# Kernel tuning notes

Hardware: AMD Instinct MI355X
Metric: run time of the kernel (lower is better)

## Reference

```python
import jax, jax.numpy as jnp
import numpy as np

COUNT_BINS = 8
BOUND = 3.0
MIN_BIN_WIDTH = 1e-3
MIN_BIN_HEIGHT = 1e-3
MIN_DERIVATIVE = 1e-3
EPS = 1e-6


def _made_masks(D, H1, H2, M):
    indeg = np.arange(1, D + 1)                     # input degrees 1..D
    h1 = np.arange(H1) % (D - 1) + 1                # hidden degrees in [1, D-1]
    h2 = np.arange(H2) % (D - 1) + 1
    outdeg = np.tile(indeg, M)                      # (M*D,), reshape-compatible with (M, D)
    m1 = (h1[:, None] >= indeg[None, :]).astype(np.float32)   # (H1, D)
    m2 = (h2[:, None] >= h1[None, :]).astype(np.float32)      # (H2, H1)
    m3 = (outdeg[:, None] > h2[None, :]).astype(np.float32)   # (M*D, H2)
    return jnp.asarray(m1), jnp.asarray(m2), jnp.asarray(m3)


def _rq_spline_forward(x, w, h, d):
    # x: (B, D); w, h: (B, D, K) simplex weights; d: (B, D, K-1) softplus'd interior derivatives
    K = w.shape[-1]
    left, right = -BOUND, BOUND

    widths = MIN_BIN_WIDTH + (1.0 - MIN_BIN_WIDTH * K) * w
    heights = MIN_BIN_HEIGHT + (1.0 - MIN_BIN_HEIGHT * K) * h
    derivs = MIN_DERIVATIVE + d
    ones = jnp.ones_like(derivs[..., :1])
    derivs = jnp.concatenate([ones, derivs, ones], -1)          # (B, D, K+1), boundary slope 1

    cw = jnp.cumsum(widths, -1)
    edge_l = jnp.full_like(cw[..., :1], left)
    edge_r = jnp.full_like(cw[..., :1], right)
    cumw = jnp.concatenate([edge_l, left + (right - left) * cw[..., :-1], edge_r], -1)  # (B, D, K+1)
    widths = cumw[..., 1:] - cumw[..., :-1]
    ch = jnp.cumsum(heights, -1)
    cumh = jnp.concatenate([edge_l, left + (right - left) * ch[..., :-1], edge_r], -1)
    heights = cumh[..., 1:] - cumh[..., :-1]

    inside = (x >= left) & (x <= right)
    xc = jnp.clip(x, left, right)
    # pyro: bin_idx = sum(x >= cumwidths + eps) - 1
    idx = jnp.sum((xc[..., None] >= (cumw + EPS)).astype(jnp.int32), -1) - 1
    idx = jnp.clip(idx, 0, K - 1)                               # (B, D)

    def g(t):
        return jnp.take_along_axis(t, idx[..., None], axis=-1)[..., 0]

    x_k, w_k = g(cumw), g(widths)
    y_k, h_k = g(cumh), g(heights)
    delta = h_k / w_k
    d_k, d_k1 = g(derivs), g(derivs[..., 1:])

    theta = (xc - x_k) / w_k
    tt = theta * (1.0 - theta)
    num = h_k * (delta * theta ** 2 + d_k * tt)
    den = delta + (d_k + d_k1 - 2.0 * delta) * tt
    y = y_k + num / den
    dnum = delta ** 2 * (d_k1 * theta ** 2 + 2.0 * delta * tt + d_k * (1.0 - theta) ** 2)
    ld = jnp.log(dnum) - 2.0 * jnp.log(den)
    return jnp.where(inside, y, x), jnp.where(inside, ld, jnp.zeros_like(ld))


def _forward(x, W1, b1, W2, b2, W3, b3):
    B, D = x.shape
    H1, H2 = W1.shape[0], W2.shape[0]
    K = COUNT_BINS
    M = 3 * K - 1
    m1, m2, m3 = _made_masks(D, H1, H2, M)
    h1 = jax.nn.relu(x @ (W1 * m1).T + b1)
    h2 = jax.nn.relu(h1 @ (W2 * m2).T + b2)
    p = (h2 @ (W3 * m3).T + b3).reshape(B, M, D)                # (B, 3K-1, D)
    w = jax.nn.softmax(jnp.swapaxes(p[:, :K, :], 1, 2), axis=-1)          # (B, D, K)
    hgt = jax.nn.softmax(jnp.swapaxes(p[:, K:2 * K, :], 1, 2), axis=-1)   # (B, D, K)
    d = jax.nn.softplus(jnp.swapaxes(p[:, 2 * K:, :], 1, 2))              # (B, D, K-1)
    z, ld = _rq_spline_forward(x, w, hgt, d)
    return z, ld.sum(-1)


def setup_inputs() -> dict:
    key = jax.random.key(0)
    ks = jax.random.split(key, 7)
    B, D, H1, H2 = 32768, 64, 64, 32
    M = 3 * COUNT_BINS - 1
    s1, s2, s3 = 1.0 / np.sqrt(D), 1.0 / np.sqrt(H1), 1.0 / np.sqrt(H2)
    return {
        "x": jax.random.normal(ks[0], (B, D), jnp.float32),
        "W1": jax.random.uniform(ks[1], (H1, D), jnp.float32, -s1, s1),
        "b1": jax.random.uniform(ks[2], (H1,), jnp.float32, -s1, s1),
        "W2": jax.random.uniform(ks[3], (H2, H1), jnp.float32, -s2, s2),
        "b2": jax.random.uniform(ks[4], (H2,), jnp.float32, -s2, s2),
        "W3": jax.random.uniform(ks[5], (M * D, H2), jnp.float32, -s3, s3),
        "b3": jax.random.uniform(ks[6], (M * D,), jnp.float32, -s3, s3),
    }


def reference(x, W1, b1, W2, b2, W3, b3):
    return _forward(x, W1, b1, W2, b2, W3, b3)
```

## Files before the change

### kernel.cpp

```cpp
#include <hip/hip_runtime.h>

#define NM 23

typedef short short8 __attribute__((ext_vector_type(8)));
typedef float f32x4 __attribute__((ext_vector_type(4)));

__device__ __forceinline__ float softplus_f(float v) {
  return fmaxf(v, 0.f) + __logf(1.f + __expf(-fabsf(v)));
}

__device__ __forceinline__ float fastrcp(float v) {
  return __builtin_amdgcn_rcpf(v);
}

__device__ __forceinline__ unsigned short bf16_rne(float x) {
  unsigned u = __float_as_uint(x);
  u += 0x7FFFu + ((u >> 16) & 1u);
  return (unsigned short)(u >> 16);
}

__global__ __launch_bounds__(256) void prep_kernel(
    const float* __restrict__ W1, const float* __restrict__ W2,
    const float* __restrict__ W3,
    unsigned short* __restrict__ B1hi, unsigned short* __restrict__ B1lo,
    unsigned short* __restrict__ B2hi, unsigned short* __restrict__ B2lo,
    unsigned short* __restrict__ B3hi, unsigned short* __restrict__ B3lo) {
  const int idx = blockIdx.x * 256 + threadIdx.x;
  const int j = idx & 7, lane = (idx >> 3) & 63;
  const int col = lane & 15, quad = lane >> 4;

  if (idx < 4096) {
    const int rest = idx >> 9, kt = rest & 1, nt = rest >> 1;
    const int k = kt * 32 + quad * 8 + j;
    const int n = nt * 16 + col;
    const float v = ((n % 63) >= k) ? W1[n * 64 + k] : 0.f;
    const unsigned short h = bf16_rne(v);
    B1hi[idx] = h;
    B1lo[idx] = bf16_rne(v - __uint_as_float(((unsigned)h) << 16));
  }
  if (idx < 2048) {
    const int rest = idx >> 9, kt = rest & 1, nt = rest >> 1;
    const int k = kt * 32 + quad * 8 + j;
    const int n = nt * 16 + col;
    const float v = ((k % 63) <= n) ? W2[n * 64 + k] : 0.f;
    const unsigned short h = bf16_rne(v);
    B2hi[idx] = h;
    B2lo[idx] = bf16_rne(v - __uint_as_float(((unsigned)h) << 16));
  }
  if (idx < 92 * 64 * 8) {
    const int nt = idx >> 9;
    const int n = nt * 16 + col;
    const int d = n & 63;
    const int k = quad * 8 + j;
    const float v = (k < d) ? W3[(size_t)n * 32 + k] : 0.f;
    const unsigned short h = bf16_rne(v);
    B3hi[idx] = h;
    B3lo[idx] = bf16_rne(v - __uint_as_float(((unsigned)h) << 16));
  }
}

__device__ __forceinline__ void cvt_hilo(const float* src, short8& hi,
                                         short8& lo) {
  const f32x4 a0 = *reinterpret_cast<const f32x4*>(src);
  const f32x4 a1 = *reinterpret_cast<const f32x4*>(src + 4);
  const float af[8] = {a0.x, a0.y, a0.z, a0.w, a1.x, a1.y, a1.z, a1.w};
  #pragma unroll
  for (int j = 0; j < 8; ++j) {
    const unsigned short h = bf16_rne(af[j]);
    hi[j] = (short)h;
    lo[j] = (short)bf16_rne(af[j] - __uint_as_float(((unsigned)h) << 16));
  }
}

__global__ __launch_bounds__(256, 4) void fused_kernel(
    const float* __restrict__ x,
    const unsigned short* __restrict__ B1hi,
    const unsigned short* __restrict__ B1lo,
    const float* __restrict__ b1,
    const unsigned short* __restrict__ B2hi,
    const unsigned short* __restrict__ B2lo,
    const float* __restrict__ b2,
    const unsigned short* __restrict__ B3hi,
    const unsigned short* __restrict__ B3lo,
    const float* __restrict__ b3,
    float* __restrict__ out, int B) {
  __shared__ float xs[64][68];
  __shared__ float h2s[64][36];
  __shared__ float b3s[64 * NM];

  const int t = threadIdx.x;
  const int b0 = blockIdx.x * 64;

  #pragma unroll
  for (int u = 0; u < 4; ++u) {
    const int idx = t + u * 256;
    const int rr = idx >> 4, c4 = (idx & 15) * 4;
    const float4 v = *reinterpret_cast<const float4*>(
        x + (size_t)b0 * 64 + (size_t)idx * 4);
    xs[rr][c4 + 0] = v.x; xs[rr][c4 + 1] = v.y;
    xs[rr][c4 + 2] = v.z; xs[rr][c4 + 3] = v.w;
  }
  for (int idx = t; idx < 64 * NM; idx += 256) {
    const int dl = idx / NM, m = idx - dl * NM;
    b3s[idx] = b3[m * 64 + dl];
  }
  __syncthreads();

  const int lane = t & 63;
  const int wv   = __builtin_amdgcn_readfirstlane(t >> 6);
  const int mt   = wv;
  const int col  = lane & 15;
  const int quad = lane >> 4;
  const int arow = mt * 16 + col;
  const int row0 = mt * 16 + quad * 4;

  float xvv[4][4];
  #pragma unroll
  for (int dc = 0; dc < 4; ++dc)
    #pragma unroll
    for (int reg = 0; reg < 4; ++reg)
      xvv[dc][reg] = xs[row0 + reg][dc * 16 + col];

  {
    short8 ahi[2], alo[2];
    #pragma unroll
    for (int kt = 0; kt < 2; ++kt)
      cvt_hilo(&xs[arow][kt * 32 + quad * 8], ahi[kt], alo[kt]);

    #pragma unroll
    for (int nt = 0; nt < 4; ++nt) {
      const float bv = b1[nt * 16 + col];
      f32x4 acc = {bv, bv, bv, bv};
      #pragma unroll
      for (int kt = 0; kt < 2; ++kt) {
        const size_t off = ((size_t)(nt * 2 + kt) * 64 + lane) * 8;
        const short8 bh = *reinterpret_cast<const short8*>(B1hi + off);
        const short8 bl = *reinterpret_cast<const short8*>(B1lo + off);
        acc = __builtin_amdgcn_mfma_f32_16x16x32_bf16(ahi[kt], bh, acc, 0, 0, 0);
        acc = __builtin_amdgcn_mfma_f32_16x16x32_bf16(alo[kt], bh, acc, 0, 0, 0);
        acc = __builtin_amdgcn_mfma_f32_16x16x32_bf16(ahi[kt], bl, acc, 0, 0, 0);
      }
      #pragma unroll
      for (int reg = 0; reg < 4; ++reg)
        xs[row0 + reg][nt * 16 + col] = fmaxf(acc[reg], 0.f);
    }
  }

  {
    short8 ahi[2], alo[2];
    #pragma unroll
    for (int kt = 0; kt < 2; ++kt)
      cvt_hilo(&xs[arow][kt * 32 + quad * 8], ahi[kt], alo[kt]);

    #pragma unroll
    for (int nt = 0; nt < 2; ++nt) {
      const float bv = b2[nt * 16 + col];
      f32x4 acc = {bv, bv, bv, bv};
      #pragma unroll
      for (int kt = 0; kt < 2; ++kt) {
        const size_t off = ((size_t)(nt * 2 + kt) * 64 + lane) * 8;
        const short8 bh = *reinterpret_cast<const short8*>(B2hi + off);
        const short8 bl = *reinterpret_cast<const short8*>(B2lo + off);
        acc = __builtin_amdgcn_mfma_f32_16x16x32_bf16(ahi[kt], bh, acc, 0, 0, 0);
        acc = __builtin_amdgcn_mfma_f32_16x16x32_bf16(alo[kt], bh, acc, 0, 0, 0);
        acc = __builtin_amdgcn_mfma_f32_16x16x32_bf16(ahi[kt], bl, acc, 0, 0, 0);
      }
      #pragma unroll
      for (int reg = 0; reg < 4; ++reg)
        h2s[row0 + reg][nt * 16 + col] = fmaxf(acc[reg], 0.f);
    }
  }

  short8 ahi, alo;
  cvt_hilo(&h2s[arow][quad * 8], ahi, alo);

  float ldr[4] = {0.f, 0.f, 0.f, 0.f};
  const float WSC = 1.0f - 1e-3f * 8.0f;

  #pragma unroll 1
  for (int dc = 0; dc < 4; ++dc) {
    const int d = dc * 16 + col;

    float xcv[4], fidx[4], xkv[4], wkv[4], ykv[4], hkv[4];

    {
      f32x4 acc[8];
      #pragma unroll
      for (int m = 0; m < 8; ++m) {
        const float bv = b3s[d * NM + m];
        acc[m] = (f32x4){bv, bv, bv, bv};
      }
      #pragma unroll
      for (int m = 0; m < 8; ++m) {
        const size_t off = ((size_t)(4 * m + dc) * 64 + lane) * 8;
        const short8 bh = *reinterpret_cast<const short8*>(B3hi + off);
        const short8 bl = *reinterpret_cast<const short8*>(B3lo + off);
        acc[m] = __builtin_amdgcn_mfma_f32_16x16x32_bf16(ahi, bh, acc[m], 0, 0, 0);
        acc[m] = __builtin_amdgcn_mfma_f32_16x16x32_bf16(alo, bh, acc[m], 0, 0, 0);
        acc[m] = __builtin_amdgcn_mfma_f32_16x16x32_bf16(ahi, bl, acc[m], 0, 0, 0);
      }
      #pragma unroll
      for (int reg = 0; reg < 4; ++reg) {
        float ew[8], sw = 0.f;
        #pragma unroll
        for (int k = 0; k < 8; ++k) { ew[k] = __expf(acc[k][reg]); sw += ew[k]; }
        const float invw = fastrcp(sw);
        float cumw[9];
        cumw[0] = -3.f;
        float cw = 0.f;
        #pragma unroll
        for (int k = 0; k < 7; ++k) {
          cw += 1e-3f + WSC * (ew[k] * invw);
          cumw[k + 1] = fmaf(6.f, cw, -3.f);
        }
        cumw[8] = 3.f;

        const float xv = xvv[dc][reg];
        const float xc = fminf(fmaxf(xv, -3.f), 3.f);
        float fi = 0.f, xk = cumw[0], xk1 = cumw[1];
        #pragma unroll
        for (int k = 1; k < 8; ++k) {
          const bool s = xc >= cumw[k] + 1e-6f;
          xk  = s ? cumw[k]     : xk;
          xk1 = s ? cumw[k + 1] : xk1;
          fi  = s ? (float)k    : fi;
        }
        xcv[reg] = xc; fidx[reg] = fi; xkv[reg] = xk; wkv[reg] = xk1 - xk;
      }
    }

    {
      f32x4 acc[8];
      #pragma unroll
      for (int m = 0; m < 8; ++m) {
        const float bv = b3s[d * NM + (8 + m)];
        acc[m] = (f32x4){bv, bv, bv, bv};
      }
      #pragma unroll
      for (int m = 0; m < 8; ++m) {
        const size_t off = ((size_t)(4 * (8 + m) + dc) * 64 + lane) * 8;
        const short8 bh = *reinterpret_cast<const short8*>(B3hi + off);
        const short8 bl = *reinterpret_cast<const short8*>(B3lo + off);
        acc[m] = __builtin_amdgcn_mfma_f32_16x16x32_bf16(ahi, bh, acc[m], 0, 0, 0);
        acc[m] = __builtin_amdgcn_mfma_f32_16x16x32_bf16(alo, bh, acc[m], 0, 0, 0);
        acc[m] = __builtin_amdgcn_mfma_f32_16x16x32_bf16(ahi, bl, acc[m], 0, 0, 0);
      }
      #pragma unroll
      for (int reg = 0; reg < 4; ++reg) {
        float eh[8], sh = 0.f;
        #pragma unroll
        for (int k = 0; k < 8; ++k) { eh[k] = __expf(acc[k][reg]); sh += eh[k]; }
        const float invh = fastrcp(sh);
        float cumh[9];
        cumh[0] = -3.f;
        float ch = 0.f;
        #pragma unroll
        for (int k = 0; k < 7; ++k) {
          ch += 1e-3f + WSC * (eh[k] * invh);
          cumh[k + 1] = fmaf(6.f, ch, -3.f);
        }
        cumh[8] = 3.f;

        float yk = cumh[0], yk1 = cumh[1];
        #pragma unroll
        for (int k = 1; k < 8; ++k) {
          const bool s = fidx[reg] >= (float)k;
          yk  = s ? cumh[k]     : yk;
          yk1 = s ? cumh[k + 1] : yk1;
        }
        ykv[reg] = yk; hkv[reg] = yk1 - yk;
      }
    }

    {
      f32x4 acc[7];
      #pragma unroll
      for (int m = 0; m < 7; ++m) {
        const float bv = b3s[d * NM + (16 + m)];
        acc[m] = (f32x4){bv, bv, bv, bv};
      }
      #pragma unroll
      for (int m = 0; m < 7; ++m) {
        const size_t off = ((size_t)(4 * (16 + m) + dc) * 64 + lane) * 8;
        const short8 bh = *reinterpret_cast<const short8*>(B3hi + off);
        const short8 bl = *reinterpret_cast<const short8*>(B3lo + off);
        acc[m] = __builtin_amdgcn_mfma_f32_16x16x32_bf16(ahi, bh, acc[m], 0, 0, 0);
        acc[m] = __builtin_amdgcn_mfma_f32_16x16x32_bf16(alo, bh, acc[m], 0, 0, 0);
        acc[m] = __builtin_amdgcn_mfma_f32_16x16x32_bf16(ahi, bl, acc[m], 0, 0, 0);
      }
      #pragma unroll
      for (int reg = 0; reg < 4; ++reg) {
        float p[7];
        #pragma unroll
        for (int k = 0; k < 7; ++k) p[k] = acc[k][reg];
        const float fi = fidx[reg];

        float pa = p[0], pb = p[0];
        #pragma unroll
        for (int k = 2; k < 8; ++k) pa = (fi >= (float)k) ? p[k - 1] : pa;
        #pragma unroll
        for (int k = 1; k < 7; ++k) pb = (fi >= (float)k) ? p[k] : pb;
        const float spa = 1e-3f + softplus_f(pa);
        const float spb = 1e-3f + softplus_f(pb);
        const float dk  = (fi >= 0.5f) ? spa : 1.f;
        const float dk1 = (fi >= 6.5f) ? 1.f : spb;

        const float xc = xcv[reg], xk = xkv[reg], wk = wkv[reg];
        const float yk = ykv[reg], hk = hkv[reg];
        const float invwk = fastrcp(wk);
        const float delta = hk * invwk;
        const float theta = (xc - xk) * invwk;
        const float omt = 1.f - theta;
        const float tt = theta * omt;
        const float th2 = theta * theta;
        const float num = hk * (delta * th2 + dk * tt);
        const float den = delta + (dk + dk1 - 2.f * delta) * tt;
        const float rden = fastrcp(den);
        const float yv = yk + num * rden;
        const float dnum =
            delta * delta * (dk1 * th2 + 2.f * delta * tt + dk * omt * omt);
        const float ldv = __logf(dnum * rden * rden);

        const float xv = xvv[dc][reg];
        const bool inside = (xv >= -3.f) && (xv <= 3.f);
        xs[row0 + reg][d] = inside ? yv : xv;
        ldr[reg] += inside ? ldv : 0.f;
      }
    }
  }

  #pragma unroll
  for (int mask = 1; mask <= 8; mask <<= 1) {
    #pragma unroll
    for (int reg = 0; reg < 4; ++reg)
      ldr[reg] += __shfl_xor(ldr[reg], mask, 64);
  }

  if (col == 0) {
    #pragma unroll
    for (int reg = 0; reg < 4; ++reg)
      out[(size_t)B * 64 + b0 + row0 + reg] = ldr[reg];
  }

  __syncthreads();

  #pragma unroll
  for (int u = 0; u < 4; ++u) {
    const int idx = t + u * 256;
    const int rr = idx >> 4, c4 = (idx & 15) * 4;
    const float4 v = make_float4(xs[rr][c4 + 0], xs[rr][c4 + 1],
                                 xs[rr][c4 + 2], xs[rr][c4 + 3]);
    *reinterpret_cast<float4*>(out + (size_t)(b0 + rr) * 64 + c4) = v;
  }
}

extern "C" void kernel_launch(void* const* d_in, const int* in_sizes, int n_in,
                              void* d_out, int out_size, void* d_ws, size_t ws_size,
                              hipStream_t stream) {
  const float* x  = (const float*)d_in[0];
  const float* W1 = (const float*)d_in[1];
  const float* b1 = (const float*)d_in[2];
  const float* W2 = (const float*)d_in[3];
  const float* b2 = (const float*)d_in[4];
  const float* W3 = (const float*)d_in[5];
  const float* b3 = (const float*)d_in[6];
  float* out = (float*)d_out;
  char* ws   = (char*)d_ws;

  unsigned short* B1hi = (unsigned short*)(ws);
  unsigned short* B1lo = (unsigned short*)(ws + 8192);
  unsigned short* B2hi = (unsigned short*)(ws + 16384);
  unsigned short* B2lo = (unsigned short*)(ws + 20480);
  unsigned short* B3hi = (unsigned short*)(ws + 24576);
  unsigned short* B3lo = (unsigned short*)(ws + 118784);

  const int B = in_sizes[0] / 64;

  prep_kernel<<<184, 256, 0, stream>>>(W1, W2, W3, B1hi, B1lo, B2hi, B2lo,
                                       B3hi, B3lo);

  fused_kernel<<<B / 64, 256, 0, stream>>>(
      x, B1hi, B1lo, b1, B2hi, B2lo, b2, B3hi, B3lo, b3, out, B);
}
```

Measured before the change: 117.5 us.

## Split spline feature dimension across two blocks per row tile with logdet reduce kernel

Launches twice as many blocks: each block recomputes layers 1-2 for its 64 rows but handles only half of the 64 output features in the costly layer-3 and spline stage. Per-half log-determinants go to a workspace and are summed by a new small reduce kernel. The aim is more parallelism and a shorter per-block tail, at the cost of doing the first two layers twice, reading x twice, and an extra launch.

```diff
diff --git a/kernel.cpp b/kernel.cpp
--- a/kernel.cpp
+++ b/kernel.cpp
@@ -83,13 +83,16 @@
     const unsigned short* __restrict__ B3hi,
     const unsigned short* __restrict__ B3lo,
     const float* __restrict__ b3,
-    float* __restrict__ out, int B) {
+    float* __restrict__ out, float* __restrict__ ldws, int B) {
   __shared__ float xs[64][68];
   __shared__ float h2s[64][36];
-  __shared__ float b3s[64 * NM];
+  __shared__ float b3s[32 * NM];
 
   const int t = threadIdx.x;
-  const int b0 = blockIdx.x * 64;
+  const int bid = blockIdx.x;
+  const int ds = (bid >> 3) & 1;
+  const int rb = ((bid >> 4) << 3) | (bid & 7);
+  const int b0 = rb * 64;
 
   #pragma unroll
   for (int u = 0; u < 4; ++u) {
@@ -100,9 +103,9 @@
     xs[rr][c4 + 0] = v.x; xs[rr][c4 + 1] = v.y;
     xs[rr][c4 + 2] = v.z; xs[rr][c4 + 3] = v.w;
   }
-  for (int idx = t; idx < 64 * NM; idx += 256) {
+  for (int idx = t; idx < 32 * NM; idx += 256) {
     const int dl = idx / NM, m = idx - dl * NM;
-    b3s[idx] = b3[m * 64 + dl];
+    b3s[idx] = b3[m * 64 + ds * 32 + dl];
   }
   __syncthreads();
 
@@ -114,12 +117,12 @@
   const int arow = mt * 16 + col;
   const int row0 = mt * 16 + quad * 4;
 
-  float xvv[4][4];
-  #pragma unroll
-  for (int dc = 0; dc < 4; ++dc)
+  float xvv[2][4];
+  #pragma unroll
+  for (int dcl = 0; dcl < 2; ++dcl)
     #pragma unroll
     for (int reg = 0; reg < 4; ++reg)
-      xvv[dc][reg] = xs[row0 + reg][dc * 16 + col];
+      xvv[dcl][reg] = xs[row0 + reg][ds * 32 + dcl * 16 + col];
 
   {
     short8 ahi[2], alo[2];
@@ -178,8 +181,9 @@
   const float WSC = 1.0f - 1e-3f * 8.0f;
 
   #pragma unroll 1
-  for (int dc = 0; dc < 4; ++dc) {
-    const int d = dc * 16 + col;
+  for (int dcl = 0; dcl < 2; ++dcl) {
+    const int dc = ds * 2 + dcl;
+    const int dl = dcl * 16 + col;
 
     float xcv[4], fidx[4], xkv[4], wkv[4], ykv[4], hkv[4];
 
@@ -187,7 +191,7 @@
       f32x4 acc[8];
       #pragma unroll
       for (int m = 0; m < 8; ++m) {
-        const float bv = b3s[d * NM + m];
+        const float bv = b3s[dl * NM + m];
         acc[m] = (f32x4){bv, bv, bv, bv};
       }
       #pragma unroll
@@ -215,7 +219,7 @@
         }
         cumw[8] = 3.f;
 
-        const float xv = xvv[dc][reg];
+        const float xv = xvv[dcl][reg];
         const float xc = fminf(fmaxf(xv, -3.f), 3.f);
         float fi = 0.f, xk = cumw[0], xk1 = cumw[1];
         #pragma unroll
@@ -233,7 +237,7 @@
       f32x4 acc[8];
       #pragma unroll
       for (int m = 0; m < 8; ++m) {
-        const float bv = b3s[d * NM + (8 + m)];
+        const float bv = b3s[dl * NM + (8 + m)];
         acc[m] = (f32x4){bv, bv, bv, bv};
       }
       #pragma unroll
@@ -276,7 +280,7 @@
       f32x4 acc[7];
       #pragma unroll
       for (int m = 0; m < 7; ++m) {
-        const float bv = b3s[d * NM + (16 + m)];
+        const float bv = b3s[dl * NM + (16 + m)];
         acc[m] = (f32x4){bv, bv, bv, bv};
       }
       #pragma unroll
@@ -321,9 +325,9 @@
             delta * delta * (dk1 * th2 + 2.f * delta * tt + dk * omt * omt);
         const float ldv = __logf(dnum * rden * rden);
 
-        const float xv = xvv[dc][reg];
+        const float xv = xvv[dcl][reg];
         const bool inside = (xv >= -3.f) && (xv <= 3.f);
-        xs[row0 + reg][d] = inside ? yv : xv;
+        h2s[row0 + reg][dl] = inside ? yv : xv;
         ldr[reg] += inside ? ldv : 0.f;
       }
     }
@@ -339,19 +343,26 @@
   if (col == 0) {
     #pragma unroll
     for (int reg = 0; reg < 4; ++reg)
-      out[(size_t)B * 64 + b0 + row0 + reg] = ldr[reg];
+      ldws[(size_t)ds * B + b0 + row0 + reg] = ldr[reg];
   }
 
   __syncthreads();
 
   #pragma unroll
-  for (int u = 0; u < 4; ++u) {
+  for (int u = 0; u < 2; ++u) {
     const int idx = t + u * 256;
-    const int rr = idx >> 4, c4 = (idx & 15) * 4;
-    const float4 v = make_float4(xs[rr][c4 + 0], xs[rr][c4 + 1],
-                                 xs[rr][c4 + 2], xs[rr][c4 + 3]);
-    *reinterpret_cast<float4*>(out + (size_t)(b0 + rr) * 64 + c4) = v;
-  }
+    const int rr = idx >> 3, c4 = (idx & 7) * 4;
+    const float4 v = make_float4(h2s[rr][c4 + 0], h2s[rr][c4 + 1],
+                                 h2s[rr][c4 + 2], h2s[rr][c4 + 3]);
+    *reinterpret_cast<float4*>(
+        out + (size_t)(b0 + rr) * 64 + ds * 32 + c4) = v;
+  }
+}
+
+__global__ __launch_bounds__(256) void ld_reduce(
+    const float* __restrict__ ldws, float* __restrict__ out, int B) {
+  const int idx = blockIdx.x * 256 + threadIdx.x;
+  if (idx < B) out[(size_t)B * 64 + idx] = ldws[idx] + ldws[B + idx];
 }
 
 extern "C" void kernel_launch(void* const* d_in, const int* in_sizes, int n_in,
@@ -373,12 +384,15 @@
   unsigned short* B2lo = (unsigned short*)(ws + 20480);
   unsigned short* B3hi = (unsigned short*)(ws + 24576);
   unsigned short* B3lo = (unsigned short*)(ws + 118784);
+  float* ldws = (float*)(ws + 212992);
 
   const int B = in_sizes[0] / 64;
 
   prep_kernel<<<184, 256, 0, stream>>>(W1, W2, W3, B1hi, B1lo, B2hi, B2lo,
                                        B3hi, B3lo);
 
-  fused_kernel<<<B / 64, 256, 0, stream>>>(
-      x, B1hi, B1lo, b1, B2hi, B2lo, b2, B3hi, B3lo, b3, out, B);
-}
+  fused_kernel<<<(B / 64) * 2, 256, 0, stream>>>(
+      x, B1hi, B1lo, b1, B2hi, B2lo, b2, B3hi, B3lo, b3, out, ldws, B);
+
+  ld_reduce<<<(B + 255) / 256, 256, 0, stream>>>(ldws, out, B);
+}
```

Measured after the change: 108.7 us. 7.5% less time.
